# Optimization experiments

Measured on AMD Instinct MI355X. Metric: run time of the kernel, lower is better.

Reference implementation:

```python
import jax, jax.numpy as jnp
import numpy as np

B, H, W, C, NB = 3, 256, 256, 16, 4
EPS = 1e-3  # keras BatchNormalization default epsilon


def _conv(x, w, b):
    y = jax.lax.conv_general_dilated(x, w, (1, 1), 'SAME',
                                     dimension_numbers=('NHWC', 'HWIO', 'NHWC'))
    return y + b


def _bn(x, g, be, mu, v):
    # inference-mode batch norm with moving statistics
    return (x - mu) * jax.lax.rsqrt(v + EPS) * g + be


def _extract_patches(x, p, s):
    # tf.image.extract_patches(..., padding='SAME') -> (b, oh, ow, p, p, c)
    b, h, w, c = x.shape
    oh, ow = -(-h // s), -(-w // s)
    pth = max((oh - 1) * s + p - h, 0)
    ptw = max((ow - 1) * s + p - w, 0)
    xp = jnp.pad(x, ((0, 0), (pth // 2, pth - pth // 2), (ptw // 2, ptw - ptw // 2), (0, 0)))
    ri = np.arange(oh)[:, None] * s + np.arange(p)[None, :]  # (oh, p)
    ci = np.arange(ow)[:, None] * s + np.arange(p)[None, :]  # (ow, p)
    return xp[:, ri[:, None, :, None], ci[None, :, None, :], :]


def setup_inputs() -> dict:
    key = jax.random.key(0)
    ks = jax.random.split(key, 4)
    mr = jax.random.normal(ks[0], (B, H, W, C), jnp.float32)
    pet = jax.random.normal(ks[1], (B, H, W, C), jnp.float32)
    W1 = jax.random.normal(ks[2], (3, 3, C, C * NB), jnp.float32) * 0.05
    W2 = jax.random.normal(ks[3], (3, 3, C * NB, C * NB), jnp.float32) * 0.05
    z = jnp.zeros((C * NB,), jnp.float32)
    o = jnp.ones((C * NB,), jnp.float32)
    return dict(mr_features=mr, pet_features=pet,
                W1=W1, b1=z, g1=o, be1=z, mu1=z, v1=o,
                W2=W2, b2=z, g2=o, be2=z, mu2=z, v2=o,
                patch=8, stride=4)


def reference(mr_features, pet_features, W1, b1, g1, be1, mu1, v1,
              W2, b2, g2, be2, mu2, v2, patch, stride):
    px = py = int(patch)
    sx = sy = int(stride)
    bsz, h, w, c = mr_features.shape

    # ---- B_Kernel_Function_Generator ----
    x = jax.nn.relu(_bn(_conv(mr_features, W1, b1), g1, be1, mu1, v1))
    x = _bn(_conv(x, W2, b2), g2, be2, mu2, v2)  # last conv_block: no activation
    nb = x.shape[-1] // c
    x = x.reshape(bsz, h, w, c, nb)
    x = jax.nn.softmax(x, axis=-1)
    b_features = jnp.where(x > 1e-5, x, 0.0)  # mask * x

    # ---- Sparse_Kernel_Matrix_Multiplication ----
    bc, bf = c, nb
    Nx, Ny = h // px, w // py
    lx, ly = px // sx, py // sy
    SNx, SNy = Nx * lx, Ny * ly

    bflat = b_features.reshape(bsz, h, w, bc * bf)
    bp = _extract_patches(bflat, px, sx).reshape(bsz, SNx, SNy, px, py, bc, bf)
    pp = _extract_patches(pet_features, px, sx).reshape(bsz, SNx, SNy, px, py, bc, 1)

    dn = jnp.sum(bp, axis=(3, 4), keepdims=True)              # diagonal norm
    kp = jnp.sum(pp * bp, axis=(3, 4), keepdims=True)         # kernel-weighted PET
    dn_safe = jnp.where(dn == 0, 1.0, dn)
    kn = jnp.where(dn == 0, 0.0, kp / dn_safe) * bp           # divide_no_nan
    kpet = jnp.sum(kn, axis=-1)                               # (b,SNx,SNy,px,py,bc)

    # deinterleave stride phases: kernel_pet[:, i::lx, j::ly] stack
    kp6 = kpet.reshape(bsz, Nx, lx, Ny, ly, px, py, c)
    st = kp6.transpose(4, 2, 0, 1, 3, 5, 6, 7).reshape(lx * ly, bsz, Nx, Ny, px, py, c)
    t = st.transpose(1, 2, 3, 4, 5, 6, 0).reshape(bsz, Nx, Ny, px, py, c, lx, ly)
    t = t.transpose(0, 1, 3, 2, 4, 5, 6, 7).reshape(bsz, Nx * px, Ny * py, c, lx, ly)
    t = t.transpose(4, 5, 0, 1, 2, 3)  # (lx, ly, b, H, W, c)

    # align_patches: roll each shifted copy back into registration, then mean
    rev = t.transpose(2, 3, 4, 5, 0, 1).reshape(bsz, h, w, c, lx * ly)
    rev = rev.transpose(4, 0, 1, 2, 3)  # (lx*ly, b, H, W, c)
    rollx = np.arange(-px // 2 + sx // 2, px // 2 + sx // 2, sx)
    rolly = np.arange(-py // 2 + sy // 2, py // 2 + sy // 2, sy)
    acc = jnp.zeros((bsz, h, w, c), rev.dtype)
    for m in range(lx * ly):  # small fixed set (lx*ly = 4)
        acc = acc + jnp.roll(rev[m], (int(rollx[m % lx]), int(rolly[m // lx])), axis=(1, 2))
    return acc / (lx * ly)
```

## Files before the change

kernel.cpp:

```cpp
#include <hip/hip_runtime.h>

#define EPSB 1e-3f

typedef _Float16 half8 __attribute__((ext_vector_type(8)));
typedef _Float16 half4 __attribute__((ext_vector_type(4)));
typedef float f32x4 __attribute__((ext_vector_type(4)));

__global__ __launch_bounds__(256, 4)
void k_prep(const float* __restrict__ W1, const float* __restrict__ W2,
            const float* __restrict__ b1, const float* __restrict__ g1,
            const float* __restrict__ be1, const float* __restrict__ mu1,
            const float* __restrict__ v1,
            const float* __restrict__ b2, const float* __restrict__ g2,
            const float* __restrict__ be2, const float* __restrict__ mu2,
            const float* __restrict__ v2,
            _Float16* __restrict__ W1F, _Float16* __restrict__ W2F,
            float* __restrict__ ST)
{
    int t = blockIdx.x * 256 + threadIdx.x;
    if (t < 5 * 4 * 64 * 8) {
        int k = t & 7, lane = (t >> 3) & 63, snt = t >> 9;
        int s = snt >> 2, ct = snt & 3;
        int quad = lane >> 4, n16 = lane & 15;
        int tap = 2 * s + (quad >> 1);
        int ci  = (quad & 1) * 8 + k;
        int co  = ct * 16 + n16;
        float v = (tap < 9) ? W1[(tap * 16 + ci) * 64 + co] : 0.f;
        W1F[t] = (_Float16)v;
        return;
    }
    t -= 5 * 4 * 64 * 8;
    if (t < 18 * 4 * 64 * 8) {
        int k = t & 7, lane = (t >> 3) & 63, snt = t >> 9;
        int s = snt >> 2, ct = snt & 3;
        int quad = lane >> 4, n16 = lane & 15;
        int tap = s >> 1;
        int ci  = (s & 1) * 32 + quad * 8 + k;
        int co  = ct * 16 + n16;
        W2F[t] = (_Float16)W2[(tap * 64 + ci) * 64 + co];
        return;
    }
    t -= 18 * 4 * 64 * 8;
    if (t < 256) {
        int c = t & 63, sel = t >> 6;
        if (sel == 0)      ST[c]       = g1[c] * rsqrtf(v1[c] + EPSB);
        else if (sel == 1) ST[64 + c]  = (b1[c] - mu1[c]) * (g1[c] * rsqrtf(v1[c] + EPSB)) + be1[c];
        else if (sel == 2) ST[128 + c] = g2[c] * rsqrtf(v2[c] + EPSB);
        else               ST[192 + c] = (b2[c] - mu2[c]) * (g2[c] * rsqrtf(v2[c] + EPSB)) + be2[c];
    }
}

#define CIPM 20
__global__ __launch_bounds__(256, 3)
void k_convf(const float* __restrict__ mr, const _Float16* __restrict__ W1F,
             const _Float16* __restrict__ W2F, const float* __restrict__ ST,
             const float* __restrict__ pet,
             _Float16* __restrict__ BF, float* __restrict__ S2)
{
    __shared__ __align__(16) _Float16 sMR[8192];
    __shared__ __align__(16) _Float16 sC1[4 * 66 * 64];
    _Float16* const sBF = sMR;
    const int tid = threadIdx.x;
    const int b  = blockIdx.y;
    const int r0 = (blockIdx.x >> 2) * 2;
    const int q0 = (blockIdx.x & 3) * 64;

    for (int idx = tid; idx < 6 * 68 * 2; idx += 256) {
        int c = idx & 1, pp = idx >> 1;
        int p = pp % 68, dys = pp / 68;
        int rr = r0 + dys - 2, qg = q0 + p - 2;
        half8 h = (half8)(_Float16)0.f;
        if ((unsigned)rr < 256u && (unsigned)qg < 256u) {
            const float* src = mr + ((b * 256 + rr) * 256 + qg) * 16 + c * 8;
            float4 v0 = *(const float4*)src;
            float4 v1 = *(const float4*)(src + 4);
            h = (half8){(_Float16)v0.x, (_Float16)v0.y, (_Float16)v0.z, (_Float16)v0.w,
                        (_Float16)v1.x, (_Float16)v1.y, (_Float16)v1.z, (_Float16)v1.w};
        }
        *(half8*)(&sMR[pp * CIPM + c * 8]) = h;
    }
    __syncthreads();

    const int w = tid >> 6, lane = tid & 63;
    const int n16 = lane & 15, quad = lane >> 4;

    {
        const _Float16* Wl1 = W1F + lane * 8;
        const int ci0 = (quad & 1) * 8;
        #pragma unroll
        for (int k = 0; k < 5; ++k) {
            const int g  = w + 4 * k;
            const int y  = g / 5;
            const int xi = g % 5;
            const int x0 = xi * 13 - ((xi >> 2) << 1);
            const int px = x0 + n16;

            f32x4 a1[4];
            #pragma unroll
            for (int ct = 0; ct < 4; ++ct) a1[ct] = (f32x4){0.f, 0.f, 0.f, 0.f};

            half8 wf1[2][4], pf1[2];
            auto load1 = [&](int s, int buf) {
                int tap  = 2 * s + (quad >> 1);
                int tapc = tap > 8 ? 8 : tap;
                int dy = tapc / 3, dx = tapc % 3;
                #pragma unroll
                for (int ct = 0; ct < 4; ++ct)
                    wf1[buf][ct] = *(const half8*)(Wl1 + (s * 4 + ct) * 512);
                pf1[buf] = *(const half8*)&sMR[((y + dy) * 68 + px + dx) * CIPM + ci0];
            };
            load1(0, 0);
            load1(1, 1);
            #pragma unroll
            for (int s = 0; s < 5; ++s) {
                const int buf = s & 1;
                #pragma unroll
                for (int ct = 0; ct < 4; ++ct)
                    a1[ct] = __builtin_amdgcn_mfma_f32_16x16x32_f16(wf1[buf][ct], pf1[buf], a1[ct], 0, 0, 0);
                if (s + 2 < 5) load1(s + 2, buf);
            }

            const bool valid = ((unsigned)(r0 - 1 + y) < 256u) && ((unsigned)(q0 - 1 + px) < 256u);
            #pragma unroll
            for (int ct = 0; ct < 4; ++ct) {
                int co0 = ct * 16 + quad * 4;
                f32x4 sc = *(const f32x4*)&ST[co0];
                f32x4 sh = *(const f32x4*)&ST[64 + co0];
                half4 h;
                #pragma unroll
                for (int j = 0; j < 4; ++j)
                    h[j] = (_Float16)fmaxf(a1[ct][j] * sc[j] + sh[j], 0.f);
                if (!valid) h = (half4)(_Float16)0.f;
                int slot = ct * 2 + (quad >> 1);
                *(half4*)&sC1[(y * 66 + px) * 64 + ((slot ^ (px & 7)) << 3) + (quad & 1) * 4] = h;
            }
        }
    }
    __syncthreads();

    const int ctw = w;
    const _Float16* Wl = W2F + lane * 8;

    f32x4 acc[2][4];
    #pragma unroll
    for (int i = 0; i < 2; ++i)
        #pragma unroll
        for (int j = 0; j < 4; ++j) acc[i][j] = (f32x4){0.f, 0.f, 0.f, 0.f};

    half8 wfb[8];
    half8 pfb[2][2][4];
    auto loadw = [&](int s, int buf) {
        wfb[buf] = *(const half8*)(Wl + (s * 4 + ctw) * 512);
    };
    auto loadp = [&](int s, int buf) {
        const int tap = s >> 1;
        const int dy = tap / 3, dx = tap % 3;
        const int slot = (s & 1) * 4 + quad;
        const int sxm = (n16 + dx) & 7;
        #pragma unroll
        for (int rr = 0; rr < 2; ++rr)
            #pragma unroll
            for (int qt = 0; qt < 4; ++qt)
                pfb[buf][rr][qt] = *(const half8*)&sC1[((rr + dy) * 66 + qt * 16 + n16 + dx) * 64 + ((slot ^ sxm) << 3)];
    };
    loadw(0, 0); loadw(1, 1); loadw(2, 2); loadw(3, 3);
    loadw(4, 4); loadw(5, 5); loadw(6, 6); loadw(7, 7);
    loadp(0, 0); loadp(1, 1);
    #pragma unroll
    for (int s = 0; s < 18; ++s) {
        const int bw = s & 7, bp = s & 1;
        #pragma unroll
        for (int rr = 0; rr < 2; ++rr)
            #pragma unroll
            for (int qt = 0; qt < 4; ++qt)
                acc[rr][qt] = __builtin_amdgcn_mfma_f32_16x16x32_f16(wfb[bw], pfb[bp][rr][qt], acc[rr][qt], 0, 0, 0);
        if (s + 8 < 18) loadw(s + 8, bw);
        if (s + 2 < 18) loadp(s + 2, bp);
    }

    half4 hv[2][4];
    {
        const int co0 = ctw * 16 + quad * 4;
        f32x4 sc = *(const f32x4*)&ST[128 + co0];
        f32x4 sh = *(const f32x4*)&ST[192 + co0];
        #pragma unroll
        for (int rr = 0; rr < 2; ++rr)
            #pragma unroll
            for (int qt = 0; qt < 4; ++qt) {
                float z0 = acc[rr][qt][0] * sc[0] + sh[0];
                float z1 = acc[rr][qt][1] * sc[1] + sh[1];
                float z2 = acc[rr][qt][2] * sc[2] + sh[2];
                float z3 = acc[rr][qt][3] * sc[3] + sh[3];
                float mx = fmaxf(fmaxf(z0, z1), fmaxf(z2, z3));
                float e0 = __expf(z0 - mx), e1 = __expf(z1 - mx);
                float e2 = __expf(z2 - mx), e3 = __expf(z3 - mx);
                float inv = __builtin_amdgcn_rcpf((e0 + e1) + (e2 + e3));
                float p0 = e0 * inv, p1 = e1 * inv, p2 = e2 * inv, p3 = e3 * inv;
                half4 h;
                h[0] = (_Float16)(p0 > 1e-5f ? p0 : 0.f);
                h[1] = (_Float16)(p1 > 1e-5f ? p1 : 0.f);
                h[2] = (_Float16)(p2 > 1e-5f ? p2 : 0.f);
                h[3] = (_Float16)(p3 > 1e-5f ? p3 : 0.f);
                hv[rr][qt] = h;
            }
    }

    {
        const int slotw = ctw * 2 + (quad >> 1);
        const int sub   = (quad & 1) * 4;
        #pragma unroll
        for (int rr = 0; rr < 2; ++rr)
            #pragma unroll
            for (int qt = 0; qt < 4; ++qt) {
                int ql = qt * 16 + n16;
                *(half4*)(&sBF[(rr * 64 + ql) * 64 + ((slotw ^ (ql & 7)) << 3) + sub]) = hv[rr][qt];
            }
    }
    __syncthreads();

    for (int idx = tid; idx < 1024; idx += 256) {
        int rl2 = idx >> 9, rest = idx & 511;
        int ql = rest >> 3, seg = rest & 7;
        int4 v = *(const int4*)&sBF[(rl2 * 64 + ql) * 64 + ((seg ^ (ql & 7)) << 3)];
        *(int4*)(BF + (((b * 256 + r0 + rl2) * 256 + q0 + ql) * 64 + seg * 8)) = v;
    }

    const int qp = tid >> 3, chg = tid & 7;
    {
        float dn[8], kp[8];
        #pragma unroll
        for (int j = 0; j < 8; ++j) { dn[j] = 0.f; kp[j] = 0.f; }
        #pragma unroll
        for (int u = 0; u < 2; ++u)
            #pragma unroll
            for (int v = 0; v < 2; ++v) {
                int rl = u, ql = 2 * qp + v;
                half8 bf = *(const half8*)(&sBF[(rl * 64 + ql) * 64 + ((chg ^ (ql & 7)) << 3)]);
                float2 p2 = *(const float2*)(pet + ((b * 256 + r0 + rl) * 256 + q0 + ql) * 16 + chg * 2);
                #pragma unroll
                for (int j = 0; j < 8; ++j) {
                    float bv = (float)bf[j];
                    dn[j] += bv;
                    kp[j] = fmaf((j < 4) ? p2.x : p2.y, bv, kp[j]);
                }
            }
        float* o = S2 + 2 * ((size_t)(((b * 128 + (r0 >> 1)) * 128 + (q0 >> 1) + qp) * 64) + chg * 8);
        #pragma unroll
        for (int m = 0; m < 4; ++m)
            *(float4*)(o + 4 * m) = make_float4(dn[2*m], kp[2*m], dn[2*m+1], kp[2*m+1]);
    }
}

__global__ __launch_bounds__(256, 8)
void k_ratio(const float* __restrict__ S2, float* __restrict__ RATIO)
{
    int t = blockIdx.x * 256 + threadIdx.x;
    int cf = t & 63;
    int j2 = (t >> 6) & 31;
    int i  = (t >> 11) & 63;
    int b  = t >> 17;
    float dn0 = 0.f, kp0 = 0.f, dn1 = 0.f, kp1 = 0.f;
    #pragma unroll
    for (int u = 0; u < 4; ++u) {
        int r2 = 2 * i - 1 + u;
        if ((unsigned)r2 >= 128u) continue;
        const float* rowp = S2 + 2 * (((size_t)(b * 128 + r2) * 128) * 64 + cf);
        float2 sv[6];
        #pragma unroll
        for (int tq = 0; tq < 6; ++tq) {
            int q2 = 4 * j2 - 1 + tq;
            sv[tq] = ((unsigned)q2 < 128u) ? *(const float2*)(rowp + q2 * 128)
                                           : make_float2(0.f, 0.f);
        }
        dn0 += sv[0].x; kp0 += sv[0].y;
        dn0 += sv[1].x; kp0 += sv[1].y;
        dn0 += sv[2].x; kp0 += sv[2].y;
        dn0 += sv[3].x; kp0 += sv[3].y;
        dn1 += sv[2].x; kp1 += sv[2].y;
        dn1 += sv[3].x; kp1 += sv[3].y;
        dn1 += sv[4].x; kp1 += sv[4].y;
        dn1 += sv[5].x; kp1 += sv[5].y;
    }
    size_t base = ((size_t)(b * 64 + i) * 64 + 2 * j2) * 64 + cf;
    RATIO[base]      = (dn0 == 0.f) ? 0.f : 0.25f * kp0 * __builtin_amdgcn_rcpf(dn0);
    RATIO[base + 64] = (dn1 == 0.f) ? 0.f : 0.25f * kp1 * __builtin_amdgcn_rcpf(dn1);
}

__global__ __launch_bounds__(256, 4)
void k_out(const _Float16* __restrict__ BF, const float* __restrict__ RATIO,
           float* __restrict__ out)
{
    __shared__ __align__(16) float sU[64 * 68];
    const int tid = threadIdx.x;
    const int g = blockIdx.x % 65;
    const int b = blockIdx.x / 65;
    const int rf = (g == 0) ? 0 : 4 * g - 2;
    const int nr = (g == 0 || g == 64) ? 2 : 4;

    const int i0 = (rf <= 253) ? 2 * ((rf + 2) >> 3)       : -1;
    const int i1 = (rf >= 2)   ? 2 * ((rf - 2) >> 3) + 1   : -1;

    for (int idx = tid; idx < 1024; idx += 256) {
        int j = idx >> 4, c4 = idx & 15;
        float4 a = make_float4(0.f, 0.f, 0.f, 0.f);
        if (i0 >= 0) a = *(const float4*)&RATIO[(((b * 64 + i0) * 64 + j) << 6) + 4 * c4];
        float4 bb = make_float4(0.f, 0.f, 0.f, 0.f);
        if (i1 >= 0) bb = *(const float4*)&RATIO[(((b * 64 + i1) * 64 + j) << 6) + 4 * c4];
        *(float4*)&sU[j * 68 + 4 * c4] = make_float4(a.x + bb.x, a.y + bb.y, a.z + bb.z, a.w + bb.w);
    }
    __syncthreads();

    const int q = tid;
    const int j0 = (q <= 253) ? 2 * ((q + 2) >> 3)     : -1;
    const int j1 = (q >= 2)   ? 2 * ((q - 2) >> 3) + 1 : -1;

    for (int rr = 0; rr < nr; ++rr) {
        const int r = rf + rr;
        const half8* bfp = (const half8*)(BF + ((size_t)(b * 256 + r) * 256 + q) * 64);
        float o[16];
        #pragma unroll
        for (int c = 0; c < 16; ++c) o[c] = 0.f;

        #pragma unroll
        for (int c2 = 0; c2 < 8; ++c2) {
            half8 bf8 = bfp[c2];
            float s0 = 0.f, s1 = 0.f;
            #pragma unroll
            for (int pj = 0; pj < 2; ++pj) {
                int jj = pj ? j1 : j0;
                if (jj < 0) continue;
                const float* up = &sU[jj * 68 + 8 * c2];
                s0 += (float)bf8[0] * up[0] + (float)bf8[1] * up[1]
                    + (float)bf8[2] * up[2] + (float)bf8[3] * up[3];
                s1 += (float)bf8[4] * up[4] + (float)bf8[5] * up[5]
                    + (float)bf8[6] * up[6] + (float)bf8[7] * up[7];
            }
            o[2 * c2]     = s0;
            o[2 * c2 + 1] = s1;
        }
        float* op = out + ((size_t)(b * 256 + r) * 256 + q) * 16;
        #pragma unroll
        for (int m = 0; m < 4; ++m)
            *(float4*)(op + 4 * m) = make_float4(o[4*m], o[4*m+1], o[4*m+2], o[4*m+3]);
    }
}

extern "C" void kernel_launch(void* const* d_in, const int* in_sizes, int n_in,
                              void* d_out, int out_size, void* d_ws, size_t ws_size,
                              hipStream_t stream) {
    const float* mr  = (const float*)d_in[0];
    const float* pet = (const float*)d_in[1];
    const float* W1  = (const float*)d_in[2];
    const float* b1  = (const float*)d_in[3];
    const float* g1  = (const float*)d_in[4];
    const float* be1 = (const float*)d_in[5];
    const float* mu1 = (const float*)d_in[6];
    const float* v1  = (const float*)d_in[7];
    const float* W2  = (const float*)d_in[8];
    const float* b2  = (const float*)d_in[9];
    const float* g2  = (const float*)d_in[10];
    const float* be2 = (const float*)d_in[11];
    const float* mu2 = (const float*)d_in[12];
    const float* v2  = (const float*)d_in[13];

    char* ws = (char*)d_ws;
    _Float16* BF    = (_Float16*)(ws);
    float*    S2    = (float*)(ws + 25165824);
    float*    RATIO = (float*)(ws + 50331648);
    _Float16* W1F   = (_Float16*)(ws + 53477376);
    _Float16* W2F   = (_Float16*)(ws + 53497856);
    float*    ST    = (float*)(ws + 53571584);
    float*    out   = (float*)d_out;

    dim3 blk(256);
    k_prep<<<185, blk, 0, stream>>>(W1, W2, b1, g1, be1, mu1, v1,
                                    b2, g2, be2, mu2, v2, W1F, W2F, ST);
    k_convf<<<dim3(512, 3), blk, 0, stream>>>(mr, W1F, W2F, ST, pet, BF, S2);
    k_ratio<<<1536, blk, 0, stream>>>(S2, RATIO);
    k_out<<<195, blk, 0, stream>>>(BF, RATIO, out);
}
```

Before: 160.0 us.

## Drop shared-memory staging of input and output tiles in fused conv kernel

The first conv now reads the mr input straight from global memory into registers, with triple-buffered prefetch, instead of staging a padded fp16 tile in LDS. The B-feature output is written directly from registers. The 2x2 pooled dn/kp sums are computed in registers using a cross-lane shuffle rather than re-reading an LDS copy. This removes the sMR buffer and two block barriers, cuts LDS use enough to raise the launch-bounds occupancy target from 3 to 4 blocks, and drops the LDS round trips. The cost is redundant, less coalesced global loads of mr across taps, uncoalesced half4 stores to BF, and scalar pet loads.

```diff
diff --git a/kernel.cpp b/kernel.cpp
--- a/kernel.cpp
+++ b/kernel.cpp
@@ -50,36 +50,17 @@
     }
 }
 
-#define CIPM 20
-__global__ __launch_bounds__(256, 3)
+__global__ __launch_bounds__(256, 4)
 void k_convf(const float* __restrict__ mr, const _Float16* __restrict__ W1F,
              const _Float16* __restrict__ W2F, const float* __restrict__ ST,
              const float* __restrict__ pet,
              _Float16* __restrict__ BF, float* __restrict__ S2)
 {
-    __shared__ __align__(16) _Float16 sMR[8192];
     __shared__ __align__(16) _Float16 sC1[4 * 66 * 64];
-    _Float16* const sBF = sMR;
     const int tid = threadIdx.x;
     const int b  = blockIdx.y;
     const int r0 = (blockIdx.x >> 2) * 2;
     const int q0 = (blockIdx.x & 3) * 64;
-
-    for (int idx = tid; idx < 6 * 68 * 2; idx += 256) {
-        int c = idx & 1, pp = idx >> 1;
-        int p = pp % 68, dys = pp / 68;
-        int rr = r0 + dys - 2, qg = q0 + p - 2;
-        half8 h = (half8)(_Float16)0.f;
-        if ((unsigned)rr < 256u && (unsigned)qg < 256u) {
-            const float* src = mr + ((b * 256 + rr) * 256 + qg) * 16 + c * 8;
-            float4 v0 = *(const float4*)src;
-            float4 v1 = *(const float4*)(src + 4);
-            h = (half8){(_Float16)v0.x, (_Float16)v0.y, (_Float16)v0.z, (_Float16)v0.w,
-                        (_Float16)v1.x, (_Float16)v1.y, (_Float16)v1.z, (_Float16)v1.w};
-        }
-        *(half8*)(&sMR[pp * CIPM + c * 8]) = h;
-    }
-    __syncthreads();
 
     const int w = tid >> 6, lane = tid & 63;
     const int n16 = lane & 15, quad = lane >> 4;
@@ -99,25 +80,36 @@
             #pragma unroll
             for (int ct = 0; ct < 4; ++ct) a1[ct] = (f32x4){0.f, 0.f, 0.f, 0.f};
 
-            half8 wf1[2][4], pf1[2];
-            auto load1 = [&](int s, int buf) {
+            half8 wf1[2][4], pf1[3];
+            auto loadw1 = [&](int s, int buf) {
+                #pragma unroll
+                for (int ct = 0; ct < 4; ++ct)
+                    wf1[buf][ct] = *(const half8*)(Wl1 + (s * 4 + ct) * 512);
+            };
+            auto loadp1 = [&](int s, int buf) {
                 int tap  = 2 * s + (quad >> 1);
                 int tapc = tap > 8 ? 8 : tap;
                 int dy = tapc / 3, dx = tapc % 3;
+                int rr = r0 + y + dy - 2, qg = q0 + px + dx - 2;
+                half8 h = (half8)(_Float16)0.f;
+                if ((unsigned)rr < 256u && (unsigned)qg < 256u) {
+                    const float* src = mr + ((b * 256 + rr) * 256 + qg) * 16 + ci0;
+                    float4 v0 = *(const float4*)src;
+                    float4 v1 = *(const float4*)(src + 4);
+                    h = (half8){(_Float16)v0.x, (_Float16)v0.y, (_Float16)v0.z, (_Float16)v0.w,
+                                (_Float16)v1.x, (_Float16)v1.y, (_Float16)v1.z, (_Float16)v1.w};
+                }
+                pf1[buf] = h;
+            };
+            loadw1(0, 0); loadw1(1, 1);
+            loadp1(0, 0); loadp1(1, 1); loadp1(2, 2);
+            #pragma unroll
+            for (int s = 0; s < 5; ++s) {
                 #pragma unroll
                 for (int ct = 0; ct < 4; ++ct)
-                    wf1[buf][ct] = *(const half8*)(Wl1 + (s * 4 + ct) * 512);
-                pf1[buf] = *(const half8*)&sMR[((y + dy) * 68 + px + dx) * CIPM + ci0];
-            };
-            load1(0, 0);
-            load1(1, 1);
-            #pragma unroll
-            for (int s = 0; s < 5; ++s) {
-                const int buf = s & 1;
-                #pragma unroll
-                for (int ct = 0; ct < 4; ++ct)
-                    a1[ct] = __builtin_amdgcn_mfma_f32_16x16x32_f16(wf1[buf][ct], pf1[buf], a1[ct], 0, 0, 0);
-                if (s + 2 < 5) load1(s + 2, buf);
+                    a1[ct] = __builtin_amdgcn_mfma_f32_16x16x32_f16(wf1[s & 1][ct], pf1[s % 3], a1[ct], 0, 0, 0);
+                if (s + 2 < 5) loadw1(s + 2, s & 1);
+                if (s + 3 < 5) loadp1(s + 3, s % 3);
             }
 
             const bool valid = ((unsigned)(r0 - 1 + y) < 256u) && ((unsigned)(q0 - 1 + px) < 256u);
@@ -178,9 +170,9 @@
         if (s + 2 < 18) loadp(s + 2, bp);
     }
 
+    const int co0 = ctw * 16 + quad * 4;
     half4 hv[2][4];
     {
-        const int co0 = ctw * 16 + quad * 4;
         f32x4 sc = *(const f32x4*)&ST[128 + co0];
         f32x4 sh = *(const f32x4*)&ST[192 + co0];
         #pragma unroll
@@ -205,49 +197,36 @@
             }
     }
 
+    #pragma unroll
+    for (int rr = 0; rr < 2; ++rr)
+        #pragma unroll
+        for (int qt = 0; qt < 4; ++qt) {
+            int ql = qt * 16 + n16;
+            *(half4*)(BF + (((b * 256 + r0 + rr) * 256 + q0 + ql) * 64 + co0)) = hv[rr][qt];
+        }
+
     {
-        const int slotw = ctw * 2 + (quad >> 1);
-        const int sub   = (quad & 1) * 4;
-        #pragma unroll
-        for (int rr = 0; rr < 2; ++rr)
-            #pragma unroll
-            for (int qt = 0; qt < 4; ++qt) {
-                int ql = qt * 16 + n16;
-                *(half4*)(&sBF[(rr * 64 + ql) * 64 + ((slotw ^ (ql & 7)) << 3) + sub]) = hv[rr][qt];
-            }
-    }
-    __syncthreads();
-
-    for (int idx = tid; idx < 1024; idx += 256) {
-        int rl2 = idx >> 9, rest = idx & 511;
-        int ql = rest >> 3, seg = rest & 7;
-        int4 v = *(const int4*)&sBF[(rl2 * 64 + ql) * 64 + ((seg ^ (ql & 7)) << 3)];
-        *(int4*)(BF + (((b * 256 + r0 + rl2) * 256 + q0 + ql) * 64 + seg * 8)) = v;
-    }
-
-    const int qp = tid >> 3, chg = tid & 7;
-    {
-        float dn[8], kp[8];
-        #pragma unroll
-        for (int j = 0; j < 8; ++j) { dn[j] = 0.f; kp[j] = 0.f; }
-        #pragma unroll
-        for (int u = 0; u < 2; ++u)
-            #pragma unroll
-            for (int v = 0; v < 2; ++v) {
-                int rl = u, ql = 2 * qp + v;
-                half8 bf = *(const half8*)(&sBF[(rl * 64 + ql) * 64 + ((chg ^ (ql & 7)) << 3)]);
-                float2 p2 = *(const float2*)(pet + ((b * 256 + r0 + rl) * 256 + q0 + ql) * 16 + chg * 2);
-                #pragma unroll
-                for (int j = 0; j < 8; ++j) {
-                    float bv = (float)bf[j];
-                    dn[j] += bv;
-                    kp[j] = fmaf((j < 4) ? p2.x : p2.y, bv, kp[j]);
-                }
-            }
-        float* o = S2 + 2 * ((size_t)(((b * 128 + (r0 >> 1)) * 128 + (q0 >> 1) + qp) * 64) + chg * 8);
-        #pragma unroll
-        for (int m = 0; m < 4; ++m)
-            *(float4*)(o + 4 * m) = make_float4(dn[2*m], kp[2*m], dn[2*m+1], kp[2*m+1]);
+        const int pc = co0 >> 2;
+        #pragma unroll
+        for (int qt = 0; qt < 4; ++qt) {
+            int ql = qt * 16 + n16;
+            float p0 = pet[((b * 256 + r0 + 0) * 256 + q0 + ql) * 16 + pc];
+            float p1 = pet[((b * 256 + r0 + 1) * 256 + q0 + ql) * 16 + pc];
+            f32x4 dns, kps;
+            #pragma unroll
+            for (int j = 0; j < 4; ++j) {
+                float v0 = (float)hv[0][qt][j];
+                float v1 = (float)hv[1][qt][j];
+                float dnp = v0 + v1;
+                float kpp = fmaf(p0, v0, p1 * v1);
+                dns[j] = dnp + __shfl_xor(dnp, 1, 64);
+                kps[j] = kpp + __shfl_xor(kpp, 1, 64);
+            }
+            int cell = qt * 8 + (n16 >> 1);
+            int jb = (n16 & 1) * 2;
+            float* o = S2 + 2 * ((size_t)(((b * 128 + (r0 >> 1)) * 128 + (q0 >> 1) + cell) * 64) + co0 + jb);
+            *(float4*)o = make_float4(dns[jb], kps[jb], dns[jb + 1], kps[jb + 1]);
+        }
     }
 }
 
```

Measured after the change: 266.0 us. 66.3% more time.
